# Performance work log

Hardware: AMD Instinct MI355X
Metric: run time of the kernel (lower is better)

Reference implementation:

```python
import jax, jax.numpy as jnp
import numpy as np

# RWKV6 layer dims (from init_kwargs + fla defaults)
H, DK, DV, NH = 512, 256, 512, 4          # hidden, key_dim, value_dim, heads
HK, HV = DK // NH, DV // NH               # 64, 128
RLOW, WLOW, ID = 32, 64, 1024             # proj_low_rank, decay_low_rank, ffn intermediate
EPS = 1e-5
B, T = 8, 1024


def layernorm(x, g, b):
    m = x.mean(-1, keepdims=True)
    v = ((x - m) ** 2).mean(-1, keepdims=True)
    return (x - m) * jax.lax.rsqrt(v + EPS) * g + b


def token_shift(x):  # shift sequence right by one, zero-pad first token
    return jnp.pad(x, ((0, 0), (1, 0), (0, 0)))[:, :-1]


def rwkv_forward(x, pre_g, pre_b, attn_g, attn_b, ffn_g, ffn_b,
                 xproj_mu, xproj_w1, xproj_w2, x_bias,
                 r_W, w_W1, w_W2, w_b, k_W, v_W, g_W, bonus,
                 gnorm_g, gnorm_b, o_W, fk_mu, fk_W, fv_W, fr_mu, fr_W):
    x0 = layernorm(x, pre_g, pre_b)                 # pre_norm (layer_idx == 0)
    h = layernorm(x0, attn_g, attn_b)               # attn_norm

    # ---- time-mix (RWKV6Attention) ----
    delta = token_shift(h) - h
    # low-rank data-dependent interpolation factors for r,w,k,v,g
    z = jnp.tanh(((h + delta * xproj_mu) @ xproj_w1.T).reshape(B, T, 5, RLOW))
    z = jnp.einsum('blnr,hnr->blnh', z, xproj_w2.reshape(H, 5, RLOW)) + x_bias
    zr, zw, zk, zv, zg = (z[:, :, i] for i in range(5))
    r = ((h + delta * zr) @ r_W.T).reshape(B, T, NH, HK)
    w = jnp.tanh((h + delta * zw) @ w_W1.T) @ w_W2.T + w_b   # decay LoRA
    lw = (-jnp.exp(w)).reshape(B, T, NH, HK)                 # log per-channel decay (< 0)
    k = ((h + delta * zk) @ k_W.T).reshape(B, T, NH, HK)
    v = ((h + delta * zv) @ v_W.T).reshape(B, T, NH, HV)
    g = (h + delta * zg) @ g_W.T

    # WKV6 selective-decay linear recurrence, state S: [B,NH,HK,HV]
    def step(S, inp):
        r_t, k_t, v_t, lw_t = inp
        kv = k_t[..., :, None] * v_t[..., None, :]
        o_t = jnp.einsum('bhk,bhkv->bhv', r_t, S + bonus[None, :, :, None] * kv)
        return jnp.exp(lw_t)[..., None] * S + kv, o_t

    S0 = jnp.zeros((B, NH, HK, HV), x.dtype)
    tfirst = lambda a: jnp.swapaxes(a, 0, 1)
    _, o = jax.lax.scan(step, S0, (tfirst(r), tfirst(k), tfirst(v), tfirst(lw)))
    o = jnp.swapaxes(o, 0, 1)                        # [B,T,NH,HV]

    # GroupNorm(num_heads) over value channels, then swish gate and output proj
    mu = o.mean(-1, keepdims=True)
    var = ((o - mu) ** 2).mean(-1, keepdims=True)
    o = ((o - mu) * jax.lax.rsqrt(var + EPS)).reshape(B, T, DV) * gnorm_g + gnorm_b
    a = (o * (g * jax.nn.sigmoid(g))) @ o_W.T

    res = x0 + a

    # ---- channel-mix (RWKV6FeedForward) ----
    hf = layernorm(res, ffn_g, ffn_b)
    d2 = token_shift(hf) - hf
    kk = jnp.square(jax.nn.relu((hf + d2 * fk_mu) @ fk_W.T))
    val = kk @ fv_W.T
    rec = jax.nn.sigmoid((hf + d2 * fr_mu) @ fr_W.T)
    return res + rec * val


def setup_inputs():
    key = jax.random.key(0)
    ks = iter(jax.random.split(key, 40))
    n = lambda shape, s=0.02: jax.random.normal(next(ks), shape, jnp.float32) * s
    u = lambda shape: jax.random.uniform(next(ks), shape, dtype=jnp.float32)
    return dict(
        x=jax.random.normal(next(ks), (B, T, H), jnp.float32),
        pre_g=jnp.ones(H), pre_b=jnp.zeros(H),
        attn_g=jnp.ones(H), attn_b=jnp.zeros(H),
        ffn_g=jnp.ones(H), ffn_b=jnp.zeros(H),
        xproj_mu=u((H,)), xproj_w1=n((5 * RLOW, H)), xproj_w2=n((H, 5 * RLOW)),
        x_bias=n((5, H)),
        r_W=n((DK, H)),
        w_W1=n((WLOW, H)), w_W2=n((DK, WLOW)), w_b=n((DK,), 0.5),
        k_W=n((DK, H)), v_W=n((DV, H)), g_W=n((DV, H)),
        bonus=n((NH, HK), 0.5),
        gnorm_g=jnp.ones(DV), gnorm_b=jnp.zeros(DV),
        o_W=n((H, DV)),
        fk_mu=u((H,)), fk_W=n((ID, H)),
        fv_W=n((H, ID)),
        fr_mu=u((H,)), fr_W=n((H, H)),
    )


def reference(x, pre_g, pre_b, attn_g, attn_b, ffn_g, ffn_b,
              xproj_mu, xproj_w1, xproj_w2, x_bias,
              r_W, w_W1, w_W2, w_b, k_W, v_W, g_W, bonus,
              gnorm_g, gnorm_b, o_W, fk_mu, fk_W, fv_W, fr_mu, fr_W):
    return rwkv_forward(x, pre_g, pre_b, attn_g, attn_b, ffn_g, ffn_b,
                        xproj_mu, xproj_w1, xproj_w2, x_bias,
                        r_W, w_W1, w_W2, w_b, k_W, v_W, g_W, bonus,
                        gnorm_g, gnorm_b, o_W, fk_mu, fk_W, fv_W, fr_mu, fr_W)
```

## Files before the change

kernel.cpp:

```cpp
#include <hip/hip_runtime.h>


#define DEVINL __device__ __forceinline__

constexpr int B_  = 8, T_ = 1024;
constexpr int BT_ = B_ * T_;
constexpr float EPS_ = 1e-5f;
constexpr int CH_ = 16;
constexpr int NC_ = T_ / CH_;

typedef __bf16 bf16x8 __attribute__((ext_vector_type(8)));
typedef float  f32x4  __attribute__((ext_vector_type(4)));

DEVINL unsigned short f2bs(float f) {
  union { float f; unsigned int i; } c; c.f = f;
  unsigned int x = c.i;
  return (unsigned short)((x + 0x7fffu + ((x >> 16) & 1u)) >> 16);
}
DEVINL float b2f(unsigned short u) {
  union { unsigned int i; float f; } c; c.i = ((unsigned int)u) << 16; return c.f;
}

DEVINL float block_sum256(float v, float* sb) {
  for (int o = 32; o; o >>= 1) v += __shfl_down(v, o);
  int w = threadIdx.x >> 6;
  __syncthreads();
  if ((threadIdx.x & 63) == 0) sb[w] = v;
  __syncthreads();
  return sb[0] + sb[1] + sb[2] + sb[3];
}

struct PackSeg { const float* src; int rows, cols, dst_rows; };
struct PackArgs { PackSeg s[12]; int base[13]; };

__global__ __launch_bounds__(256) void pack_kernel(PackArgs pa, unsigned short* dst)
{
  int i = blockIdx.x * 256 + threadIdx.x;
  if (i >= pa.base[12]) return;
  int k = 0;
  while (i >= pa.base[k + 1]) k++;
  int loc = i - pa.base[k];
  PackSeg s = pa.s[k];
  int r = loc / s.cols, c = loc - r * s.cols;
  float v = (r < s.rows) ? s.src[(size_t)r * s.cols + c] : 0.f;
  dst[i] = f2bs(v);
}

__global__ __launch_bounds__(256) void ln2_kernel(
    const float* __restrict__ x,
    const float* __restrict__ pg, const float* __restrict__ pb,
    const float* __restrict__ ag, const float* __restrict__ ab,
    float* __restrict__ x0, unsigned short* __restrict__ h)
{
  __shared__ float sb[4];
  size_t base = (size_t)blockIdx.x * 512;
  int tid = threadIdx.x;
  float v0 = x[base + tid], v1 = x[base + 256 + tid];
  float m = block_sum256(v0 + v1, sb) * (1.f / 512.f);
  float d0 = v0 - m, d1 = v1 - m;
  float var = block_sum256(d0 * d0 + d1 * d1, sb) * (1.f / 512.f);
  float rs = rsqrtf(var + EPS_);
  float a0 = d0 * rs * pg[tid]       + pb[tid];
  float a1 = d1 * rs * pg[tid + 256] + pb[tid + 256];
  x0[base + tid] = a0; x0[base + 256 + tid] = a1;
  float m2 = block_sum256(a0 + a1, sb) * (1.f / 512.f);
  float e0 = a0 - m2, e1 = a1 - m2;
  float var2 = block_sum256(e0 * e0 + e1 * e1, sb) * (1.f / 512.f);
  float rs2 = rsqrtf(var2 + EPS_);
  h[base + tid]       = f2bs(e0 * rs2 * ag[tid]       + ab[tid]);
  h[base + 256 + tid] = f2bs(e1 * rs2 * ag[tid + 256] + ab[tid + 256]);
}

__global__ __launch_bounds__(256) void ln1_kernel(
    const float* __restrict__ in,
    const float* __restrict__ g, const float* __restrict__ b,
    float* __restrict__ out)
{
  __shared__ float sb[4];
  size_t base = (size_t)blockIdx.x * 512;
  int tid = threadIdx.x;
  float v0 = in[base + tid], v1 = in[base + 256 + tid];
  float m = block_sum256(v0 + v1, sb) * (1.f / 512.f);
  float d0 = v0 - m, d1 = v1 - m;
  float var = block_sum256(d0 * d0 + d1 * d1, sb) * (1.f / 512.f);
  float rs = rsqrtf(var + EPS_);
  out[base + tid]       = d0 * rs * g[tid]       + b[tid];
  out[base + 256 + tid] = d1 * rs * g[tid + 256] + b[tid + 256];
}

__global__ __launch_bounds__(256) void ymix_kernel(
    const unsigned short* __restrict__ h, const float* __restrict__ mu,
    unsigned short* __restrict__ y, unsigned short* __restrict__ dl)
{
  int t = blockIdx.x, tid = threadIdx.x, tt = t & (T_ - 1);
  size_t base = (size_t)t * 512;
  for (int c = tid; c < 512; c += 256) {
    float cur  = b2f(h[base + c]);
    float prev = tt ? b2f(h[base - 512 + c]) : 0.f;
    float d = prev - cur;
    dl[base + c] = f2bs(d);
    y[base + c] = f2bs(cur + d * mu[c]);
  }
}

__global__ __launch_bounds__(256) void ffnmix_kernel(
    const float* __restrict__ hf, const float* __restrict__ fkmu,
    const float* __restrict__ frmu,
    unsigned short* __restrict__ mfk, unsigned short* __restrict__ mfr)
{
  int t = blockIdx.x, tid = threadIdx.x, tt = t & (T_ - 1);
  size_t base = (size_t)t * 512;
  for (int c = tid; c < 512; c += 256) {
    float cur  = hf[base + c];
    float prev = tt ? hf[base - 512 + c] : 0.f;
    float d = prev - cur;
    mfk[base + c] = f2bs(cur + d * fkmu[c]);
    mfr[base + c] = f2bs(cur + d * frmu[c]);
  }
}

constexpr int TPB_ = 8;
__global__ __launch_bounds__(256) void xmix5_kernel(
    const unsigned short* __restrict__ z5,
    const unsigned short* __restrict__ w2,
    const float* __restrict__ xbias,
    const unsigned short* __restrict__ h, const unsigned short* __restrict__ dl,
    unsigned short* __restrict__ m5)
{
  __shared__ float zL[TPB_][160];
  int t0 = blockIdx.x * TPB_;
  int tid = threadIdx.x;
  for (int i = tid; i < TPB_ * 160; i += 256) {
    int tt = i / 160, kk = i - tt * 160;
    zL[tt][kk] = b2f(z5[(size_t)(t0 + tt) * 192 + kk]);
  }
  __syncthreads();
  for (int half = 0; half < 2; half++) {
    int c = tid + half * 256;
    const int4* wp = (const int4*)(w2 + (size_t)c * 160);
    int4 wv[20];
#pragma unroll
    for (int q = 0; q < 20; q++) wv[q] = wp[q];
    float bia[5];
#pragma unroll
    for (int n = 0; n < 5; n++) bia[n] = xbias[n * 512 + c];
    for (int tt = 0; tt < TPB_; tt++) {
      size_t base = (size_t)(t0 + tt) * 512 + c;
      float hv = b2f(h[base]), dv = b2f(dl[base]);
#pragma unroll
      for (int n = 0; n < 5; n++) {
        float a = 0.f;
#pragma unroll
        for (int q = 0; q < 4; q++) {
          const unsigned short* u = (const unsigned short*)&wv[n * 4 + q];
          const float* z = &zL[tt][n * 32 + q * 8];
#pragma unroll
          for (int j = 0; j < 8; j++) a += b2f(u[j]) * z[j];
        }
        m5[(size_t)n * ((size_t)BT_ * 512) + base] = f2bs(hv + dv * (a + bia[n]));
      }
    }
  }
}

enum { EP_NONE_F32 = 0, EP_NONE_BF16 = 1, EP_TANH_BF16 = 2, EP_EXPEXP_F32 = 3,
       EP_RES_F32 = 4, EP_RELU2_BF16 = 5, EP_OUT2_F32 = 6 };

struct GemmDesc {
  const unsigned short* A; const unsigned short* W; void* C;
  const void* bias; const void* aux1; const void* aux2;
  int N, K, lda, ldw, ldc, epi;
};
template <int NG> struct GD { GemmDesc d[NG]; };

template <int BM, int BN, int NG>
__global__ __launch_bounds__(256) void mgemm(GD<NG> p)
{
  GemmDesc dd = p.d[blockIdx.z];
  int n0 = blockIdx.y * BN;
  if (n0 >= dd.N) return;
  int m0 = blockIdx.x * BM;
  constexpr int MFR = BM / 32, NFR = BN / 32;
  __shared__ short As[BM * 32];
  __shared__ short Ws[BN * 32];
  int tid = threadIdx.x, lane = tid & 63, wid = tid >> 6;
  int wm = wid >> 1, wn = wid & 1, lrow = lane & 15, lkg = lane >> 4;

  int arow, akg, wrow, wkg;
  if constexpr (BM == 128) { arow = tid >> 1; akg = (tid & 1) * 2; }
  else                     { arow = tid >> 2; akg = tid & 3; }
  if constexpr (BN == 128) { wrow = tid >> 1; wkg = (tid & 1) * 2; }
  else                     { wrow = tid >> 2; wkg = tid & 3; }
  int uA0 = (akg * (BM / 16) + (arow >> 4)) * 16 + (arow & 15);
  int uA1 = ((akg + 1) * (BM / 16) + (arow >> 4)) * 16 + (arow & 15);
  int uW0 = (wkg * (BN / 16) + (wrow >> 4)) * 16 + (wrow & 15);
  int uW1 = ((wkg + 1) * (BN / 16) + (wrow >> 4)) * 16 + (wrow & 15);

  f32x4 acc[MFR][NFR];
#pragma unroll
  for (int mf = 0; mf < MFR; mf++)
#pragma unroll
    for (int nf = 0; nf < NFR; nf++) acc[mf][nf] = (f32x4){0.f, 0.f, 0.f, 0.f};

  for (int kb = 0; kb < dd.K; kb += 32) {
    const int4* ap = (const int4*)(dd.A + (size_t)(m0 + arow) * dd.lda + kb + akg * 8);
    const int4* wp = (const int4*)(dd.W + (size_t)(n0 + wrow) * dd.ldw + kb + wkg * 8);
    int4 a0 = ap[0], w0 = wp[0], a1, w1;
    if constexpr (BM == 128) a1 = ap[1];
    if constexpr (BN == 128) w1 = wp[1];
    __syncthreads();
    *(int4*)&As[uA0 * 8] = a0;
    if constexpr (BM == 128) *(int4*)&As[uA1 * 8] = a1;
    *(int4*)&Ws[uW0 * 8] = w0;
    if constexpr (BN == 128) *(int4*)&Ws[uW1 * 8] = w1;
    __syncthreads();

    bf16x8 bfrag[NFR];
#pragma unroll
    for (int nf = 0; nf < NFR; nf++)
      bfrag[nf] = *(const bf16x8*)&Ws[((lkg * (BN / 16) + wn * NFR + nf) * 16 + lrow) * 8];
#pragma unroll
    for (int mf = 0; mf < MFR; mf++) {
      bf16x8 afrag = *(const bf16x8*)&As[((lkg * (BM / 16) + wm * MFR + mf) * 16 + lrow) * 8];
#pragma unroll
      for (int nf = 0; nf < NFR; nf++)
        acc[mf][nf] = __builtin_amdgcn_mfma_f32_16x16x32_bf16(
            bfrag[nf], afrag, acc[mf][nf], 0, 0, 0);
    }
  }

#pragma unroll
  for (int mf = 0; mf < MFR; mf++) {
#pragma unroll
    for (int nf = 0; nf < NFR; nf++) {
      int m  = m0 + wm * (MFR * 16) + mf * 16 + lrow;
      int nb = n0 + wn * (NFR * 16) + nf * 16 + lkg * 4;
      size_t off = (size_t)m * dd.ldc + nb;
      float c0 = acc[mf][nf][0], c1 = acc[mf][nf][1];
      float c2 = acc[mf][nf][2], c3 = acc[mf][nf][3];
      switch (dd.epi) {
        case EP_NONE_F32: {
          f32x4 v = {c0, c1, c2, c3};
          *(f32x4*)((float*)dd.C + off) = v; break;
        }
        case EP_NONE_BF16: {
          uint2 u; u.x = f2bs(c0) | ((unsigned)f2bs(c1) << 16);
          u.y = f2bs(c2) | ((unsigned)f2bs(c3) << 16);
          *(uint2*)((unsigned short*)dd.C + off) = u; break;
        }
        case EP_TANH_BF16: {
          uint2 u; u.x = f2bs(tanhf(c0)) | ((unsigned)f2bs(tanhf(c1)) << 16);
          u.y = f2bs(tanhf(c2)) | ((unsigned)f2bs(tanhf(c3)) << 16);
          *(uint2*)((unsigned short*)dd.C + off) = u; break;
        }
        case EP_EXPEXP_F32: {
          const float* bi = (const float*)dd.bias;
          f32x4 v = {expf(-expf(c0 + bi[nb + 0])), expf(-expf(c1 + bi[nb + 1])),
                     expf(-expf(c2 + bi[nb + 2])), expf(-expf(c3 + bi[nb + 3]))};
          *(f32x4*)((float*)dd.C + off) = v; break;
        }
        case EP_RES_F32: {
          f32x4 a = *(const f32x4*)((const float*)dd.aux1 + off);
          f32x4 v = {c0 + a[0], c1 + a[1], c2 + a[2], c3 + a[3]};
          *(f32x4*)((float*)dd.C + off) = v; break;
        }
        case EP_RELU2_BF16: {
          c0 = fmaxf(c0, 0.f); c1 = fmaxf(c1, 0.f);
          c2 = fmaxf(c2, 0.f); c3 = fmaxf(c3, 0.f);
          uint2 u; u.x = f2bs(c0 * c0) | ((unsigned)f2bs(c1 * c1) << 16);
          u.y = f2bs(c2 * c2) | ((unsigned)f2bs(c3 * c3) << 16);
          *(uint2*)((unsigned short*)dd.C + off) = u; break;
        }
        case EP_OUT2_F32: {
          f32x4 rs = *(const f32x4*)((const float*)dd.aux1 + off);
          f32x4 fr = *(const f32x4*)((const float*)dd.aux2 + off);
          f32x4 v = {rs[0] + (1.f / (1.f + expf(-fr[0]))) * c0,
                     rs[1] + (1.f / (1.f + expf(-fr[1]))) * c1,
                     rs[2] + (1.f / (1.f + expf(-fr[2]))) * c2,
                     rs[3] + (1.f / (1.f + expf(-fr[3]))) * c3};
          *(f32x4*)((float*)dd.C + off) = v; break;
        }
      }
    }
  }
}

__global__ __launch_bounds__(256) void rbk_kernel(
    const unsigned short* __restrict__ r, const unsigned short* __restrict__ k,
    const float* __restrict__ bonus, float* __restrict__ rbk)
{
  int t = blockIdx.x, tid = threadIdx.x;
  int hh = tid >> 6, j = tid & 63;
  size_t g = (size_t)t * 256 + hh * 64 + j;
  float p = b2f(r[g]) * b2f(k[g]) * bonus[hh * 64 + j];
  for (int o = 32; o; o >>= 1) p += __shfl_down(p, o);
  if (j == 0) rbk[(size_t)t * 4 + hh] = p;
}

__global__ __launch_bounds__(128) void wkv_pass1(
    const unsigned short* __restrict__ k, const float* __restrict__ ew,
    const unsigned short* __restrict__ v, unsigned short* __restrict__ Sl,
    float* __restrict__ Dp)
{
  __shared__ float kL[CH_][64], eL[CH_][64];
  int blk = blockIdx.x;
  int c = blk & (NC_ - 1), bh = blk >> 6;
  int b = bh >> 2, hh = bh & 3;
  int tid = threadIdx.x;
  size_t tbase = (size_t)b * T_ + (size_t)c * CH_;
  for (int idx = tid; idx < CH_ * 64; idx += 128) {
    int s = idx >> 6, j = idx & 63;
    size_t g = (tbase + s) * 256 + hh * 64 + j;
    kL[s][j] = b2f(k[g]); eL[s][j] = ew[g];
  }
  __syncthreads();
  float S[64];
#pragma unroll
  for (int j = 0; j < 64; j++) S[j] = 0.f;
  for (int s = 0; s < CH_; s++) {
    float vv = b2f(v[(tbase + s) * 512 + hh * 128 + tid]);
    const float4* e4p = (const float4*)&eL[s][0];
    const float4* k4p = (const float4*)&kL[s][0];
#pragma unroll
    for (int q = 0; q < 16; q++) {
      float4 e4 = e4p[q], k4 = k4p[q];
      S[4 * q + 0] = e4.x * S[4 * q + 0] + k4.x * vv;
      S[4 * q + 1] = e4.y * S[4 * q + 1] + k4.y * vv;
      S[4 * q + 2] = e4.z * S[4 * q + 2] + k4.z * vv;
      S[4 * q + 3] = e4.w * S[4 * q + 3] + k4.w * vv;
    }
  }
  size_t sbase = (size_t)blk * 8192;
#pragma unroll
  for (int j = 0; j < 64; j++) Sl[sbase + j * 128 + tid] = f2bs(S[j]);
  if (tid < 64) {
    float d = 1.f;
    for (int s = 0; s < CH_; s++) d *= eL[s][tid];
    Dp[(size_t)blk * 64 + tid] = d;
  }
}

__global__ __launch_bounds__(256) void wkv_scan(
    const unsigned short* __restrict__ Sl, const float* __restrict__ Dp,
    unsigned short* __restrict__ Ss)
{
  int e = blockIdx.x * 256 + threadIdx.x;
  int bh = e >> 13; int kv = e & 8191; int j = kv >> 7;
  float run = 0.f;
  for (int c = 0; c < NC_; c++) {
    size_t base = (size_t)bh * NC_ + c;
    Ss[base * 8192 + kv] = f2bs(run);
    run = Dp[base * 64 + j] * run + b2f(Sl[base * 8192 + kv]);
  }
}

__global__ __launch_bounds__(128) void wkv_pass3(
    const unsigned short* __restrict__ r, const unsigned short* __restrict__ k,
    const float* __restrict__ ew, const unsigned short* __restrict__ v,
    const float* __restrict__ rbk, const unsigned short* __restrict__ Ss,
    float* __restrict__ o)
{
  __shared__ float rL[CH_][64], kL[CH_][64], eL[CH_][64], rbL[CH_];
  int blk = blockIdx.x;
  int c = blk & (NC_ - 1), bh = blk >> 6;
  int b = bh >> 2, hh = bh & 3;
  int tid = threadIdx.x;
  size_t tbase = (size_t)b * T_ + (size_t)c * CH_;
  for (int idx = tid; idx < CH_ * 64; idx += 128) {
    int s = idx >> 6, j = idx & 63;
    size_t g = (tbase + s) * 256 + hh * 64 + j;
    rL[s][j] = b2f(r[g]); kL[s][j] = b2f(k[g]); eL[s][j] = ew[g];
  }
  if (tid < CH_) rbL[tid] = rbk[(tbase + tid) * 4 + hh];
  __syncthreads();
  float S[64];
  size_t sbase = (size_t)blk * 8192;
#pragma unroll
  for (int j = 0; j < 64; j++) S[j] = b2f(Ss[sbase + j * 128 + tid]);
  for (int s = 0; s < CH_; s++) {
    float vv = b2f(v[(tbase + s) * 512 + hh * 128 + tid]);
    float oa = rbL[s] * vv;
    const float4* r4p = (const float4*)&rL[s][0];
    const float4* e4p = (const float4*)&eL[s][0];
    const float4* k4p = (const float4*)&kL[s][0];
#pragma unroll
    for (int q = 0; q < 16; q++) {
      float4 r4 = r4p[q], e4 = e4p[q], k4 = k4p[q];
      oa += r4.x * S[4 * q + 0] + r4.y * S[4 * q + 1]
          + r4.z * S[4 * q + 2] + r4.w * S[4 * q + 3];
      S[4 * q + 0] = e4.x * S[4 * q + 0] + k4.x * vv;
      S[4 * q + 1] = e4.y * S[4 * q + 1] + k4.y * vv;
      S[4 * q + 2] = e4.z * S[4 * q + 2] + k4.z * vv;
      S[4 * q + 3] = e4.w * S[4 * q + 3] + k4.w * vv;
    }
    o[(tbase + s) * 512 + hh * 128 + tid] = oa;
  }
}

__global__ __launch_bounds__(256) void gn_gate_kernel(
    const float* __restrict__ o, const float* __restrict__ g,
    const float* __restrict__ gg, const float* __restrict__ gb,
    unsigned short* __restrict__ obf)
{
  __shared__ float ov[512], ps[64], qs[64], mh[4], vh[4];
  int t = blockIdx.x, tid = threadIdx.x;
  size_t base = (size_t)t * 512;
  ov[tid] = o[base + tid]; ov[tid + 256] = o[base + 256 + tid];
  __syncthreads();
  if (tid < 64) {
    int hh = tid >> 4, sg = tid & 15;
    const float* p = &ov[hh * 128 + sg * 8];
    float s = 0.f, q = 0.f;
    for (int i = 0; i < 8; i++) { s += p[i]; q += p[i] * p[i]; }
    ps[tid] = s; qs[tid] = q;
  }
  __syncthreads();
  if (tid < 4) {
    float s = 0.f, q = 0.f;
    for (int i = 0; i < 16; i++) { s += ps[tid * 16 + i]; q += qs[tid * 16 + i]; }
    float m = s * (1.f / 128.f);
    mh[tid] = m; vh[tid] = q * (1.f / 128.f) - m * m;
  }
  __syncthreads();
  for (int c = tid; c < 512; c += 256) {
    int hh = c >> 7;
    float nrm = (ov[c] - mh[hh]) * rsqrtf(vh[hh] + EPS_);
    float gv = g[base + c];
    float sw = gv * (1.f / (1.f + expf(-gv)));
    obf[base + c] = f2bs((nrm * gg[c] + gb[c]) * sw);
  }
}

extern "C" void kernel_launch(void* const* d_in, const int* in_sizes, int n_in,
                              void* d_out, int out_size, void* d_ws, size_t ws_size,
                              hipStream_t stream) {
  (void)in_sizes; (void)n_in; (void)out_size; (void)ws_size;
  const float* x        = (const float*)d_in[0];
  const float* pre_g    = (const float*)d_in[1];
  const float* pre_b    = (const float*)d_in[2];
  const float* attn_g   = (const float*)d_in[3];
  const float* attn_b   = (const float*)d_in[4];
  const float* ffn_g    = (const float*)d_in[5];
  const float* ffn_b    = (const float*)d_in[6];
  const float* xproj_mu = (const float*)d_in[7];
  const float* xproj_w1 = (const float*)d_in[8];
  const float* xproj_w2 = (const float*)d_in[9];
  const float* x_bias   = (const float*)d_in[10];
  const float* r_W      = (const float*)d_in[11];
  const float* w_W1     = (const float*)d_in[12];
  const float* w_W2     = (const float*)d_in[13];
  const float* w_b      = (const float*)d_in[14];
  const float* k_W      = (const float*)d_in[15];
  const float* v_W      = (const float*)d_in[16];
  const float* g_W      = (const float*)d_in[17];
  const float* bonus    = (const float*)d_in[18];
  const float* gnorm_g  = (const float*)d_in[19];
  const float* gnorm_b  = (const float*)d_in[20];
  const float* o_W      = (const float*)d_in[21];
  const float* fk_mu    = (const float*)d_in[22];
  const float* fk_W     = (const float*)d_in[23];
  const float* fv_W     = (const float*)d_in[24];
  const float* fr_mu    = (const float*)d_in[25];
  const float* fr_W     = (const float*)d_in[26];

  const size_t BTH = (size_t)BT_ * 512;
  size_t cur = 0;
  auto alloc = [&](size_t bytes) { void* p = (char*)d_ws + cur; cur += (bytes + 255) & ~(size_t)255; return p; };
  float*          x0    = (float*)alloc(BTH * 4);
  unsigned short* hbufb = (unsigned short*)alloc(BTH * 2);
  unsigned short* m5b   = (unsigned short*)alloc(5 * BTH * 2);
  unsigned short* rbuf  = (unsigned short*)alloc((size_t)BT_ * 256 * 4);
  unsigned short* kbuf  = (unsigned short*)alloc((size_t)BT_ * 256 * 4);
  float*          ebuf  = (float*)alloc((size_t)BT_ * 256 * 4);
  unsigned short* vbuf  = (unsigned short*)alloc(BTH * 4);
  float*          gbuf  = (float*)alloc(BTH * 4);
  unsigned short* wtmpb = (unsigned short*)alloc((size_t)BT_ * 128 * 2);
  float*          rbk   = (float*)alloc((size_t)BT_ * 4 * 4);
  unsigned short* Sl    = (unsigned short*)alloc((size_t)2048 * 8192 * 2);
  unsigned short* Ss    = (unsigned short*)alloc((size_t)2048 * 8192 * 2);
  float*          Dp    = (float*)alloc((size_t)2048 * 64 * 4);
  float*          res   = (float*)alloc(BTH * 4);
  unsigned short* wpack = (unsigned short*)alloc((size_t)2621440 * 2);
  unsigned short* ybufb = rbuf;
  unsigned short* dlb   = vbuf;
  unsigned short* z5b   = (unsigned short*)gbuf;
  float*          obuf  = (float*)m5b;
  unsigned short* obf16 = (unsigned short*)ebuf;
  float*          hf    = x0;
  unsigned short* mfk   = rbuf;
  unsigned short* mfr   = kbuf;
  unsigned short* kkb   = Sl;
  float*          frtmp = (float*)vbuf;

  PackArgs pa;
  int off = 0, seg = 0;
  auto addseg = [&](const float* src, int rows, int cols, int dst_rows) {
    pa.s[seg] = {src, rows, cols, dst_rows};
    pa.base[seg] = off; off += dst_rows * cols; seg++;
  };
  addseg(xproj_w1, 160, 512, 192);   int o_w1p = pa.base[0];
  addseg(w_W1,      64, 512, 128);   int o_wW1 = pa.base[1];
  addseg(r_W,      256, 512, 256);   int o_rW  = pa.base[2];
  addseg(k_W,      256, 512, 256);   int o_kW  = pa.base[3];
  addseg(v_W,      512, 512, 512);   int o_vW  = pa.base[4];
  addseg(g_W,      512, 512, 512);   int o_gW  = pa.base[5];
  addseg(o_W,      512, 512, 512);   int o_oW  = pa.base[6];
  addseg(fk_W,    1024, 512, 1024);  int o_fkW = pa.base[7];
  addseg(fv_W,     512, 1024, 512);  int o_fvW = pa.base[8];
  addseg(fr_W,     512, 512, 512);   int o_frW = pa.base[9];
  addseg(w_W2,     256, 64, 256);    int o_wW2 = pa.base[10];
  addseg(xproj_w2, 512, 160, 512);   int o_xw2 = pa.base[11];
  pa.base[12] = off;

  pack_kernel<<<(off + 255) / 256, 256, 0, stream>>>(pa, wpack);
  ln2_kernel<<<BT_, 256, 0, stream>>>(x, pre_g, pre_b, attn_g, attn_b, x0, hbufb);
  ymix_kernel<<<BT_, 256, 0, stream>>>(hbufb, xproj_mu, ybufb, dlb);

  auto solo = [&](const unsigned short* A, const unsigned short* W, void* C,
                  const void* bias, const void* a1, const void* a2,
                  int N, int K, int lda, int ldw, int ldc, int epi) {
    GD<1> g; g.d[0] = {A, W, C, bias, a1, a2, N, K, lda, ldw, ldc, epi};
    mgemm<64, 64, 1><<<dim3(128, (N + 63) / 64, 1), 256, 0, stream>>>(g);
  };

  solo(ybufb, wpack + o_w1p, z5b, nullptr, nullptr, nullptr,
       192, 512, 512, 512, 192, EP_TANH_BF16);

  xmix5_kernel<<<BT_ / TPB_, 256, 0, stream>>>(
      z5b, wpack + o_xw2, x_bias, hbufb, dlb, m5b);

  {
    GD<5> g;
    g.d[0] = {m5b + 0 * BTH, wpack + o_rW, rbuf, nullptr, nullptr, nullptr, 256, 512, 512, 512, 256, EP_NONE_BF16};
    g.d[1] = {m5b + 1 * BTH, wpack + o_wW1, wtmpb, nullptr, nullptr, nullptr, 128, 512, 512, 512, 128, EP_TANH_BF16};
    g.d[2] = {m5b + 2 * BTH, wpack + o_kW, kbuf, nullptr, nullptr, nullptr, 256, 512, 512, 512, 256, EP_NONE_BF16};
    g.d[3] = {m5b + 3 * BTH, wpack + o_vW, vbuf, nullptr, nullptr, nullptr, 512, 512, 512, 512, 512, EP_NONE_BF16};
    g.d[4] = {m5b + 4 * BTH, wpack + o_gW, gbuf, nullptr, nullptr, nullptr, 512, 512, 512, 512, 512, EP_NONE_F32};
    mgemm<128, 128, 5><<<dim3(64, 4, 5), 256, 0, stream>>>(g);
  }

  solo(wtmpb, wpack + o_wW2, ebuf, w_b, nullptr, nullptr,
       256, 64, 128, 64, 256, EP_EXPEXP_F32);

  rbk_kernel<<<BT_, 256, 0, stream>>>(rbuf, kbuf, bonus, rbk);
  wkv_pass1<<<2048, 128, 0, stream>>>(kbuf, ebuf, vbuf, Sl, Dp);
  wkv_scan<<<1024, 256, 0, stream>>>(Sl, Dp, Ss);
  wkv_pass3<<<2048, 128, 0, stream>>>(rbuf, kbuf, ebuf, vbuf, rbk, Ss, obuf);

  gn_gate_kernel<<<BT_, 256, 0, stream>>>(obuf, gbuf, gnorm_g, gnorm_b, obf16);

  solo(obf16, wpack + o_oW, res, nullptr, x0, nullptr,
       512, 512, 512, 512, 512, EP_RES_F32);

  ln1_kernel<<<BT_, 256, 0, stream>>>(res, ffn_g, ffn_b, hf);
  ffnmix_kernel<<<BT_, 256, 0, stream>>>(hf, fk_mu, fr_mu, mfk, mfr);

  {
    GD<2> g;
    g.d[0] = {mfk, wpack + o_fkW, kkb, nullptr, nullptr, nullptr, 1024, 512, 512, 512, 1024, EP_RELU2_BF16};
    g.d[1] = {mfr, wpack + o_frW, frtmp, nullptr, nullptr, nullptr, 512, 512, 512, 512, 512, EP_NONE_F32};
    mgemm<128, 128, 2><<<dim3(64, 8, 2), 256, 0, stream>>>(g);
  }

  solo(kkb, wpack + o_fvW, (float*)d_out, nullptr, res, frtmp,
       512, 1024, 1024, 1024, 512, EP_OUT2_F32);
}
```

Baseline: 361.7 us.

## Run xproj_w2 interpolation on MFMA grouped GEMM with fused mix epilogue

The scalar xmix5 kernel is replaced by five grouped MFMA GEMMs with K=32, one per interpolation factor. A new epilogue adds x_bias and computes h + delta*z in bf16 directly. The g projection output is also stored as bf16 instead of fp32, halving its write and the read in gn_gate. The K=32 GEMM barely uses a 128x128 tile and the g gate now carries bf16 rounding error.

```diff
diff --git a/kernel.cpp b/kernel.cpp
--- a/kernel.cpp
+++ b/kernel.cpp
@@ -119,52 +119,8 @@
   }
 }
 
-constexpr int TPB_ = 8;
-__global__ __launch_bounds__(256) void xmix5_kernel(
-    const unsigned short* __restrict__ z5,
-    const unsigned short* __restrict__ w2,
-    const float* __restrict__ xbias,
-    const unsigned short* __restrict__ h, const unsigned short* __restrict__ dl,
-    unsigned short* __restrict__ m5)
-{
-  __shared__ float zL[TPB_][160];
-  int t0 = blockIdx.x * TPB_;
-  int tid = threadIdx.x;
-  for (int i = tid; i < TPB_ * 160; i += 256) {
-    int tt = i / 160, kk = i - tt * 160;
-    zL[tt][kk] = b2f(z5[(size_t)(t0 + tt) * 192 + kk]);
-  }
-  __syncthreads();
-  for (int half = 0; half < 2; half++) {
-    int c = tid + half * 256;
-    const int4* wp = (const int4*)(w2 + (size_t)c * 160);
-    int4 wv[20];
-#pragma unroll
-    for (int q = 0; q < 20; q++) wv[q] = wp[q];
-    float bia[5];
-#pragma unroll
-    for (int n = 0; n < 5; n++) bia[n] = xbias[n * 512 + c];
-    for (int tt = 0; tt < TPB_; tt++) {
-      size_t base = (size_t)(t0 + tt) * 512 + c;
-      float hv = b2f(h[base]), dv = b2f(dl[base]);
-#pragma unroll
-      for (int n = 0; n < 5; n++) {
-        float a = 0.f;
-#pragma unroll
-        for (int q = 0; q < 4; q++) {
-          const unsigned short* u = (const unsigned short*)&wv[n * 4 + q];
-          const float* z = &zL[tt][n * 32 + q * 8];
-#pragma unroll
-          for (int j = 0; j < 8; j++) a += b2f(u[j]) * z[j];
-        }
-        m5[(size_t)n * ((size_t)BT_ * 512) + base] = f2bs(hv + dv * (a + bia[n]));
-      }
-    }
-  }
-}
-
 enum { EP_NONE_F32 = 0, EP_NONE_BF16 = 1, EP_TANH_BF16 = 2, EP_EXPEXP_F32 = 3,
-       EP_RES_F32 = 4, EP_RELU2_BF16 = 5, EP_OUT2_F32 = 6 };
+       EP_RES_F32 = 4, EP_RELU2_BF16 = 5, EP_OUT2_F32 = 6, EP_XMIX_BF16 = 7 };
 
 struct GemmDesc {
   const unsigned short* A; const unsigned short* W; void* C;
@@ -280,6 +236,20 @@
                      rs[3] + (1.f / (1.f + expf(-fr[3]))) * c3};
           *(f32x4*)((float*)dd.C + off) = v; break;
         }
+        case EP_XMIX_BF16: {
+          const float* bi = (const float*)dd.bias;
+          uint2 hv = *(const uint2*)((const unsigned short*)dd.aux1 + off);
+          uint2 dv = *(const uint2*)((const unsigned short*)dd.aux2 + off);
+          const unsigned short* hu = (const unsigned short*)&hv;
+          const unsigned short* du = (const unsigned short*)&dv;
+          float r0 = b2f(hu[0]) + b2f(du[0]) * (c0 + bi[nb + 0]);
+          float r1 = b2f(hu[1]) + b2f(du[1]) * (c1 + bi[nb + 1]);
+          float r2 = b2f(hu[2]) + b2f(du[2]) * (c2 + bi[nb + 2]);
+          float r3 = b2f(hu[3]) + b2f(du[3]) * (c3 + bi[nb + 3]);
+          uint2 u; u.x = f2bs(r0) | ((unsigned)f2bs(r1) << 16);
+          u.y = f2bs(r2) | ((unsigned)f2bs(r3) << 16);
+          *(uint2*)((unsigned short*)dd.C + off) = u; break;
+        }
       }
     }
   }
@@ -398,7 +368,7 @@
 }
 
 __global__ __launch_bounds__(256) void gn_gate_kernel(
-    const float* __restrict__ o, const float* __restrict__ g,
+    const float* __restrict__ o, const unsigned short* __restrict__ g,
     const float* __restrict__ gg, const float* __restrict__ gb,
     unsigned short* __restrict__ obf)
 {
@@ -425,7 +395,7 @@
   for (int c = tid; c < 512; c += 256) {
     int hh = c >> 7;
     float nrm = (ov[c] - mh[hh]) * rsqrtf(vh[hh] + EPS_);
-    float gv = g[base + c];
+    float gv = b2f(g[base + c]);
     float sw = gv * (1.f / (1.f + expf(-gv)));
     obf[base + c] = f2bs((nrm * gg[c] + gb[c]) * sw);
   }
@@ -473,7 +443,7 @@
   unsigned short* kbuf  = (unsigned short*)alloc((size_t)BT_ * 256 * 4);
   float*          ebuf  = (float*)alloc((size_t)BT_ * 256 * 4);
   unsigned short* vbuf  = (unsigned short*)alloc(BTH * 4);
-  float*          gbuf  = (float*)alloc(BTH * 4);
+  unsigned short* gbuf  = (unsigned short*)alloc(BTH * 4);
   unsigned short* wtmpb = (unsigned short*)alloc((size_t)BT_ * 128 * 2);
   float*          rbk   = (float*)alloc((size_t)BT_ * 4 * 4);
   unsigned short* Sl    = (unsigned short*)alloc((size_t)2048 * 8192 * 2);
@@ -483,7 +453,7 @@
   unsigned short* wpack = (unsigned short*)alloc((size_t)2621440 * 2);
   unsigned short* ybufb = rbuf;
   unsigned short* dlb   = vbuf;
-  unsigned short* z5b   = (unsigned short*)gbuf;
+  unsigned short* z5b   = gbuf;
   float*          obuf  = (float*)m5b;
   unsigned short* obf16 = (unsigned short*)ebuf;
   float*          hf    = x0;
@@ -526,8 +496,13 @@
   solo(ybufb, wpack + o_w1p, z5b, nullptr, nullptr, nullptr,
        192, 512, 512, 512, 192, EP_TANH_BF16);
 
-  xmix5_kernel<<<BT_ / TPB_, 256, 0, stream>>>(
-      z5b, wpack + o_xw2, x_bias, hbufb, dlb, m5b);
+  {
+    GD<5> g;
+    for (int n = 0; n < 5; n++)
+      g.d[n] = {z5b + n * 32, wpack + o_xw2 + n * 32, m5b + (size_t)n * BTH,
+                x_bias + n * 512, hbufb, dlb, 512, 32, 192, 160, 512, EP_XMIX_BF16};
+    mgemm<128, 128, 5><<<dim3(64, 4, 5), 256, 0, stream>>>(g);
+  }
 
   {
     GD<5> g;
@@ -535,7 +510,7 @@
     g.d[1] = {m5b + 1 * BTH, wpack + o_wW1, wtmpb, nullptr, nullptr, nullptr, 128, 512, 512, 512, 128, EP_TANH_BF16};
     g.d[2] = {m5b + 2 * BTH, wpack + o_kW, kbuf, nullptr, nullptr, nullptr, 256, 512, 512, 512, 256, EP_NONE_BF16};
     g.d[3] = {m5b + 3 * BTH, wpack + o_vW, vbuf, nullptr, nullptr, nullptr, 512, 512, 512, 512, 512, EP_NONE_BF16};
-    g.d[4] = {m5b + 4 * BTH, wpack + o_gW, gbuf, nullptr, nullptr, nullptr, 512, 512, 512, 512, 512, EP_NONE_F32};
+    g.d[4] = {m5b + 4 * BTH, wpack + o_gW, gbuf, nullptr, nullptr, nullptr, 512, 512, 512, 512, 512, EP_NONE_BF16};
     mgemm<128, 128, 5><<<dim3(64, 4, 5), 256, 0, stream>>>(g);
   }
 
```

After: 360.8 us. No clear change (-0.2%).
